# Performance work log

Measured on AMD Instinct MI355X. Metric: run time of the kernel, lower is better.

Reference implementation:

```python
import jax, jax.numpy as jnp
import numpy as np

T, H, I, E, S = 1024, 1024, 512, 64, 2  # tokens, hidden, intermediate, routed experts, shared experts
G, TOPK_GROUP, K = 8, 4, 8              # n_group, topk_group, num_experts_per_tok


def setup_inputs() -> dict:
    key = jax.random.key(0)
    ks = jax.random.split(key, 6)
    scale = 0.02
    x = jax.random.normal(ks[0], (T, H), dtype=jnp.float32)
    gate_w = jax.random.normal(ks[1], (E, H), dtype=jnp.float32) * scale   # MoEGate.weight [E,H]
    w_gu = jax.random.normal(ks[2], (E, H, 2 * I), dtype=jnp.float32) * scale  # gate_up_proj.weight.T per expert
    w_d = jax.random.normal(ks[3], (E, I, H), dtype=jnp.float32) * scale       # down_proj.weight.T per expert
    s_gu = jax.random.normal(ks[4], (S, H, 2 * I), dtype=jnp.float32) * scale  # shared experts
    s_d = jax.random.normal(ks[5], (S, I, H), dtype=jnp.float32) * scale
    return {"x": x, "gate_w": gate_w, "w_gu": w_gu, "w_d": w_d, "s_gu": s_gu, "s_d": s_d}


def _moe_forward(x, gate_w, w_gu, w_d, s_gu, s_d):
    t, h = x.shape
    e = w_gu.shape[0]
    i = w_gu.shape[2] // 2
    group_size = e // G

    # ---- shared experts (always active), summed ----
    sh = jnp.einsum('th,shf->stf', x, s_gu)            # [S,T,2I]
    shared = jnp.einsum('stf,sfh->th', jax.nn.silu(sh[..., :i]) * sh[..., i:], s_d)

    # ---- grouped top-k gating ----
    logits = x @ gate_w.T                               # [T,E]
    group_logits = logits.reshape(t, G, group_size)
    gw, gi = jax.lax.top_k(group_logits, TOPK_GROUP)    # [T,G,topk_group]
    gw = gw.reshape(t, G * TOPK_GROUP)
    gi = gi.reshape(t, G * TOPK_GROUP)
    topk_w, ti = jax.lax.top_k(gw, K)                   # [T,K]
    sel_group = ti // TOPK_GROUP
    expert_in_group = jnp.take_along_axis(gi, ti, axis=1)
    topk_idx = sel_group * group_size + expert_in_group # [T,K]
    topk_w = topk_w / (topk_w.sum(axis=-1, keepdims=True) + 1e-20)  # norm_topk_prob

    # ---- combine weights: sparse [T,E] scatter of top-k weights ----
    combine = jnp.zeros((t, e), x.dtype).at[jnp.arange(t)[:, None], topk_idx].add(topk_w)

    # ---- routed experts: dense grouped GEMM, zero-weighted where unselected ----
    gu = jnp.einsum('th,ehf->etf', x, w_gu)             # [E,T,2I]
    hidden = jax.nn.silu(gu[..., :i]) * gu[..., i:]     # [E,T,I]
    y = jnp.einsum('eti,eih->eth', hidden, w_d)         # [E,T,H]
    routed = jnp.einsum('eth,te->th', y, combine)

    return shared + routed


def reference(x, gate_w, w_gu, w_d, s_gu, s_d):
    return _moe_forward(x, gate_w, w_gu, w_d, s_gu, s_d)
```

## Files before the change

### kernel.cpp

```cpp
#include <hip/hip_runtime.h>
#include <hip/hip_bf16.h>

#define T_ 1024
#define H_ 1024
#define I_ 512
#define E_ 64
#define S_ 2
#define NJOB 66
#define KSEL 8
#define GRP 8
#define GSIZE 8
#define TKG 4
#define ROWS_TOTAL (T_*KSEL + S_*T_)

typedef __attribute__((ext_vector_type(8))) __bf16 bf16x8;
typedef __attribute__((ext_vector_type(8))) unsigned short u16x8;
typedef __attribute__((ext_vector_type(4))) unsigned short u16x4;
typedef __attribute__((ext_vector_type(4))) float f32x4;

__device__ inline unsigned short f2bf(float f) {
    unsigned u = __float_as_uint(f);
    u += 0x7FFFu + ((u >> 16) & 1u);
    return (unsigned short)(u >> 16);
}

__device__ inline unsigned pk2bf(float a, float b) {
    unsigned short ua = __builtin_bit_cast(unsigned short, (__bf16)a);
    unsigned short ub = __builtin_bit_cast(unsigned short, (__bf16)b);
    return (unsigned)ua | ((unsigned)ub << 16);
}

__device__ inline void async16(const void* g, void* l) {
    __builtin_amdgcn_global_load_lds(
        (const __attribute__((address_space(1))) unsigned int*)g,
        (__attribute__((address_space(3))) unsigned int*)(uintptr_t)l,
        16, 0, 0);
}

__global__ __launch_bounds__(256) void cvt_x_kernel(const float* __restrict__ x,
                                                    unsigned short* __restrict__ xb) {
    int i = (blockIdx.x * 256 + threadIdx.x) * 4;
    f32x4 v = *(const f32x4*)(x + i);
    u16x4 o;
    o[0] = f2bf(v[0]); o[1] = f2bf(v[1]); o[2] = f2bf(v[2]); o[3] = f2bf(v[3]);
    *(u16x4*)(xb + i) = o;
}

__global__ __launch_bounds__(256) void gate_kernel(const float* __restrict__ x,
                                                   const float* __restrict__ gate_w,
                                                   int* __restrict__ counts,
                                                   int* __restrict__ topk_idx,
                                                   float* __restrict__ topk_w) {
    __shared__ float Wt[64 * 65];
    __shared__ float Xs[4 * 65];
    __shared__ float lg[4 * 65];

    int tid = threadIdx.x;
    int t0 = blockIdx.x * 4;
    int e = tid & 63;
    int wq = tid >> 6;
    int er = tid >> 2;
    int kq = (tid & 3) * 16;
    int xk = tid & 63;

    float acc = 0.f;
    for (int kc = 0; kc < 16; ++kc) {
        const float* wp = gate_w + er * H_ + kc * 64 + kq;
        f32x4 w0 = *(const f32x4*)(wp);
        f32x4 w1 = *(const f32x4*)(wp + 4);
        f32x4 w2 = *(const f32x4*)(wp + 8);
        f32x4 w3 = *(const f32x4*)(wp + 12);
        float xv = x[(size_t)(t0 + wq) * H_ + kc * 64 + xk];
        __syncthreads();
#pragma unroll
        for (int i = 0; i < 4; ++i) {
            Wt[(kq + i) * 65 + er] = w0[i];
            Wt[(kq + 4 + i) * 65 + er] = w1[i];
            Wt[(kq + 8 + i) * 65 + er] = w2[i];
            Wt[(kq + 12 + i) * 65 + er] = w3[i];
        }
        Xs[wq * 65 + xk] = xv;
        __syncthreads();
#pragma unroll 8
        for (int k = 0; k < 64; ++k)
            acc += Wt[k * 65 + e] * Xs[wq * 65 + k];
    }
    lg[wq * 65 + e] = acc;
    __syncthreads();

    if (tid < 4) {
        int t = t0 + tid;
        const float* L = &lg[tid * 65];
        float cv[GRP * TKG];
        int   ce[GRP * TKG];
        for (int g = 0; g < GRP; ++g) {
            unsigned used = 0;
            for (int r = 0; r < TKG; ++r) {
                float best = -INFINITY; int bi = 0;
                for (int j = 0; j < GSIZE; ++j) {
                    if (used & (1u << j)) continue;
                    float v = L[g * GSIZE + j];
                    if (v > best) { best = v; bi = j; }
                }
                used |= 1u << bi;
                cv[g * TKG + r] = best;
                ce[g * TKG + r] = g * GSIZE + bi;
            }
        }
        float sv[KSEL]; int si[KSEL];
        unsigned used = 0;
        float sum = 0.0f;
        for (int r = 0; r < KSEL; ++r) {
            float best = -INFINITY; int bi = 0;
            for (int j = 0; j < GRP * TKG; ++j) {
                if (used & (1u << j)) continue;
                if (cv[j] > best) { best = cv[j]; bi = j; }
            }
            used |= 1u << bi;
            sv[r] = best; si[r] = ce[bi];
            sum += best;
        }
        float inv = 1.0f / (sum + 1e-20f);
        for (int r = 0; r < KSEL; ++r) {
            topk_idx[t * KSEL + r] = si[r];
            topk_w[t * KSEL + r] = sv[r] * inv;
            atomicAdd(&counts[si[r]], 1);
        }
    }
}

__global__ void prefix_kernel(int* __restrict__ counts, int* __restrict__ offsets,
                              int* __restrict__ cursor) {
    if (threadIdx.x == 0) {
        counts[E_] = T_;
        counts[E_ + 1] = T_;
        int acc = 0;
        for (int j = 0; j < NJOB; ++j) {
            offsets[j] = acc;
            cursor[j] = acc;
            acc += counts[j];
        }
        offsets[NJOB] = acc;
    }
}

__global__ __launch_bounds__(256) void place_kernel(const int* __restrict__ topk_idx,
                                                    const float* __restrict__ topk_w,
                                                    const int* __restrict__ offsets,
                                                    int* __restrict__ cursor,
                                                    int* __restrict__ row_token,
                                                    float* __restrict__ row_w) {
    int p = blockIdx.x * 256 + threadIdx.x;
    if (p < T_ * KSEL) {
        int t = p >> 3;
        int e = topk_idx[p];
        int slot = atomicAdd(&cursor[e], 1);
        row_token[slot] = t;
        row_w[slot] = topk_w[p];
    } else if (p < T_ * KSEL + S_ * T_) {
        int q = p - T_ * KSEL;
        int s = q >> 10;
        int t = q & (T_ - 1);
        int slot = offsets[E_ + s] + t;
        row_token[slot] = t;
        row_w[slot] = 1.0f;
    }
}

__global__ __launch_bounds__(256) void gateup_kernel(const unsigned short* __restrict__ xb,
                                                     const float* __restrict__ w_gu,
                                                     const float* __restrict__ s_gu,
                                                     const int* __restrict__ offsets,
                                                     const int* __restrict__ row_token,
                                                     unsigned short* __restrict__ hidden) {
    int job = blockIdx.x, mt = blockIdx.y, nt = blockIdx.z;
    int seg = offsets[job];
    int cnt = offsets[job + 1] - seg;
    int m0 = mt * 128;
    if (m0 >= cnt) return;
    const float* W = (job < E_) ? (w_gu + (size_t)job * H_ * (2 * I_))
                                : (s_gu + (size_t)(job - E_) * H_ * (2 * I_));
    int n0 = nt * 64;

    __shared__ unsigned short As[128 * 64];
    __shared__ unsigned short Bg[64 * 64];
    __shared__ unsigned short Bu[64 * 64];

    int tid = threadIdx.x;
    int wv = tid >> 6, lane = tid & 63, lrow = lane & 15, lq = lane >> 4;

    const unsigned short* asrc[4];
#pragma unroll
    for (int i = 0; i < 4; ++i) {
        int d = i * 256 + tid;
        int row = d >> 3;
        int kc = (d & 7) ^ (row & 7);
        int r = m0 + row;
        int gi = seg + (r < cnt ? r : 0);
        asrc[i] = xb + (size_t)row_token[gi] * H_ + kc * 8;
    }

    int bk = (tid & 15) * 4;
    int bn = (tid >> 4) * 4;
    int c0 = bk >> 3;
    int h8 = (bk & 4) * 2;
    const float* bbase = W + (size_t)bk * (2 * I_) + n0 + bn;

    f32x4 accg[2][4], accu[2][4];
    f32x4 zero = {0.f, 0.f, 0.f, 0.f};
#pragma unroll
    for (int a = 0; a < 2; ++a)
#pragma unroll
        for (int c = 0; c < 4; ++c) { accg[a][c] = zero; accu[a][c] = zero; }

    f32x4 g[4], u[4];
#pragma unroll
    for (int r = 0; r < 4; ++r) {
        g[r] = *(const f32x4*)(bbase + (size_t)r * (2 * I_));
        u[r] = *(const f32x4*)(bbase + (size_t)r * (2 * I_) + I_);
    }

    for (int kt = 0; kt < H_ / 64; ++kt) {
        int ko = kt * 64;
#pragma unroll
        for (int i = 0; i < 4; ++i)
            async16(asrc[i] + ko, &As[(i * 256 + tid) * 8]);

#pragma unroll
        for (int j = 0; j < 4; ++j) {
            int nj = bn + j;
            int byteoff = nj * 128 + ((c0 ^ (nj & 7)) * 16) + h8;
            uint2 vg, vu;
            vg.x = pk2bf(g[0][j], g[1][j]); vg.y = pk2bf(g[2][j], g[3][j]);
            vu.x = pk2bf(u[0][j], u[1][j]); vu.y = pk2bf(u[2][j], u[3][j]);
            *(uint2*)((char*)Bg + byteoff) = vg;
            *(uint2*)((char*)Bu + byteoff) = vu;
        }

        {
            int kn = ((kt + 1) & 15) * 64;
            const float* bp = bbase + (size_t)kn * (2 * I_);
#pragma unroll
            for (int r = 0; r < 4; ++r) {
                g[r] = *(const f32x4*)(bp + (size_t)r * (2 * I_));
                u[r] = *(const f32x4*)(bp + (size_t)r * (2 * I_) + I_);
            }
        }
        __syncthreads();

#pragma unroll
        for (int kk = 0; kk < 2; ++kk) {
            bf16x8 a[2];
#pragma unroll
            for (int rb = 0; rb < 2; ++rb) {
                int R = wv * 32 + rb * 16 + lrow;
                a[rb] = *(const bf16x8*)&As[R * 64 + (((lq + kk * 4) ^ (R & 7)) * 8)];
            }
#pragma unroll
            for (int cb = 0; cb < 4; ++cb) {
                int n = cb * 16 + lrow;
                int koff = ((lq + kk * 4) ^ (n & 7)) * 8;
                bf16x8 bg = *(const bf16x8*)&Bg[n * 64 + koff];
                bf16x8 bu = *(const bf16x8*)&Bu[n * 64 + koff];
#pragma unroll
                for (int rb = 0; rb < 2; ++rb) {
                    accg[rb][cb] = __builtin_amdgcn_mfma_f32_16x16x32_bf16(a[rb], bg, accg[rb][cb], 0, 0, 0);
                    accu[rb][cb] = __builtin_amdgcn_mfma_f32_16x16x32_bf16(a[rb], bu, accu[rb][cb], 0, 0, 0);
                }
            }
        }
        __syncthreads();
    }

#pragma unroll
    for (int rb = 0; rb < 2; ++rb)
#pragma unroll
        for (int cb = 0; cb < 4; ++cb)
#pragma unroll
            for (int r = 0; r < 4; ++r) {
                int row = wv * 32 + rb * 16 + lq * 4 + r;
                if (m0 + row < cnt) {
                    float gg = accg[rb][cb][r];
                    float uu = accu[rb][cb][r];
                    float hh = gg / (1.0f + __expf(-gg)) * uu;
                    hidden[(size_t)(seg + m0 + row) * I_ + n0 + cb * 16 + lrow] = f2bf(hh);
                }
            }
}

__global__ __launch_bounds__(256) void down_kernel(const unsigned short* __restrict__ hidden,
                                                   const float* __restrict__ w_d,
                                                   const float* __restrict__ s_d,
                                                   const int* __restrict__ offsets,
                                                   const int* __restrict__ row_token,
                                                   const float* __restrict__ row_w,
                                                   float* __restrict__ out) {
    int job = blockIdx.x, mt = blockIdx.y, nt = blockIdx.z;
    int seg = offsets[job];
    int cnt = offsets[job + 1] - seg;
    int m0 = mt * 128;
    if (m0 >= cnt) return;
    const float* W = (job < E_) ? (w_d + (size_t)job * I_ * H_)
                                : (s_d + (size_t)(job - E_) * I_ * H_);
    int n0 = nt * 64;

    __shared__ unsigned short As[128 * 64];
    __shared__ unsigned short Bs[64 * 64];

    int tid = threadIdx.x;
    int wv = tid >> 6, lane = tid & 63, lrow = lane & 15, lq = lane >> 4;

    const unsigned short* asrc[4];
#pragma unroll
    for (int i = 0; i < 4; ++i) {
        int d = i * 256 + tid;
        int row = d >> 3;
        int kc = (d & 7) ^ (row & 7);
        int r = m0 + row;
        int gi = seg + (r < cnt ? r : 0);
        asrc[i] = hidden + (size_t)gi * I_ + kc * 8;
    }

    int bk = (tid & 15) * 4;
    int bn = (tid >> 4) * 4;
    int c0 = bk >> 3;
    int h8 = (bk & 4) * 2;
    const float* bbase = W + (size_t)bk * H_ + n0 + bn;

    f32x4 acc[2][4];
    f32x4 zero = {0.f, 0.f, 0.f, 0.f};
#pragma unroll
    for (int a = 0; a < 2; ++a)
#pragma unroll
        for (int c = 0; c < 4; ++c) acc[a][c] = zero;

    f32x4 d4[4];
#pragma unroll
    for (int r = 0; r < 4; ++r)
        d4[r] = *(const f32x4*)(bbase + (size_t)r * H_);

    for (int kt = 0; kt < I_ / 64; ++kt) {
        int ko = kt * 64;
#pragma unroll
        for (int i = 0; i < 4; ++i)
            async16(asrc[i] + ko, &As[(i * 256 + tid) * 8]);

#pragma unroll
        for (int j = 0; j < 4; ++j) {
            int nj = bn + j;
            int byteoff = nj * 128 + ((c0 ^ (nj & 7)) * 16) + h8;
            uint2 vb;
            vb.x = pk2bf(d4[0][j], d4[1][j]); vb.y = pk2bf(d4[2][j], d4[3][j]);
            *(uint2*)((char*)Bs + byteoff) = vb;
        }
        {
            int kn = ((kt + 1) & 7) * 64;
            const float* bp = bbase + (size_t)kn * H_;
#pragma unroll
            for (int r = 0; r < 4; ++r)
                d4[r] = *(const f32x4*)(bp + (size_t)r * H_);
        }
        __syncthreads();

#pragma unroll
        for (int kk = 0; kk < 2; ++kk) {
            bf16x8 a[2];
#pragma unroll
            for (int rb = 0; rb < 2; ++rb) {
                int R = wv * 32 + rb * 16 + lrow;
                a[rb] = *(const bf16x8*)&As[R * 64 + (((lq + kk * 4) ^ (R & 7)) * 8)];
            }
#pragma unroll
            for (int cb = 0; cb < 4; ++cb) {
                int n = cb * 16 + lrow;
                bf16x8 b = *(const bf16x8*)&Bs[n * 64 + (((lq + kk * 4) ^ (n & 7)) * 8)];
#pragma unroll
                for (int rb = 0; rb < 2; ++rb)
                    acc[rb][cb] = __builtin_amdgcn_mfma_f32_16x16x32_bf16(a[rb], b, acc[rb][cb], 0, 0, 0);
            }
        }
        __syncthreads();
    }

#pragma unroll
    for (int rb = 0; rb < 2; ++rb)
#pragma unroll
        for (int r = 0; r < 4; ++r) {
            int row = wv * 32 + rb * 16 + lq * 4 + r;
            if (m0 + row < cnt) {
                int gi = seg + m0 + row;
                int tok = row_token[gi];
                float w = row_w[gi];
#pragma unroll
                for (int cb = 0; cb < 4; ++cb)
                    atomicAdd(&out[(size_t)tok * H_ + n0 + cb * 16 + lrow],
                              acc[rb][cb][r] * w);
            }
        }
}

extern "C" void kernel_launch(void* const* d_in, const int* in_sizes, int n_in,
                              void* d_out, int out_size, void* d_ws, size_t ws_size,
                              hipStream_t stream) {
    const float* x      = (const float*)d_in[0];
    const float* gate_w = (const float*)d_in[1];
    const float* w_gu   = (const float*)d_in[2];
    const float* w_d    = (const float*)d_in[3];
    const float* s_gu   = (const float*)d_in[4];
    const float* s_d    = (const float*)d_in[5];
    float* out = (float*)d_out;

    char* ws = (char*)d_ws;
    size_t off = 0;
    auto carve = [&](size_t bytes) -> void* {
        void* p = ws + off;
        off += (bytes + 255) & ~(size_t)255;
        return p;
    };
    int* counts            = (int*)carve(NJOB * 4);
    int* offsets           = (int*)carve((NJOB + 1) * 4);
    int* cursor            = (int*)carve(NJOB * 4);
    int* topk_idx          = (int*)carve(T_ * KSEL * 4);
    float* topk_w          = (float*)carve(T_ * KSEL * 4);
    int* row_token         = (int*)carve(ROWS_TOTAL * 4);
    float* row_w           = (float*)carve(ROWS_TOTAL * 4);
    unsigned short* xb     = (unsigned short*)carve((size_t)T_ * H_ * 2);
    unsigned short* hidden = (unsigned short*)carve((size_t)ROWS_TOTAL * I_ * 2);

    hipMemsetAsync(out, 0, (size_t)T_ * H_ * 4, stream);
    hipMemsetAsync(counts, 0, NJOB * 4, stream);

    cvt_x_kernel<<<(T_ * H_ / 4) / 256, 256, 0, stream>>>(x, xb);
    gate_kernel<<<T_ / 4, 256, 0, stream>>>(x, gate_w, counts, topk_idx, topk_w);
    prefix_kernel<<<1, 64, 0, stream>>>(counts, offsets, cursor);
    place_kernel<<<(ROWS_TOTAL + 255) / 256, 256, 0, stream>>>(topk_idx, topk_w, offsets,
                                                               cursor, row_token, row_w);
    gateup_kernel<<<dim3(NJOB, T_ / 128, I_ / 64), 256, 0, stream>>>(xb, w_gu, s_gu, offsets,
                                                                     row_token, hidden);
    down_kernel<<<dim3(NJOB, T_ / 128, H_ / 64), 256, 0, stream>>>(hidden, w_d, s_d, offsets,
                                                                   row_token, row_w, out);
}
```

Baseline: 626.3 us.

## Replace atomic scatter with per-row output buffer and reduce kernel; enlarge M tiles

The down-projection now writes unweighted per-row results to a dense yrow buffer, and a new reduce kernel gathers each token's eight routed rows plus both shared rows, applying the top-k weights. This removes the float atomicAdd scatter and the output memset. GEMM blocks grow to 256 rows with 512 threads, which halves how often each expert's weight tile is reloaded and converted. The prefix sum becomes a parallel scan. The cost is roughly 40 MB of extra yrow traffic, more LDS per block, and lower occupancy.

```diff
diff --git a/kernel.cpp b/kernel.cpp
--- a/kernel.cpp
+++ b/kernel.cpp
@@ -12,6 +12,8 @@
 #define GSIZE 8
 #define TKG 4
 #define ROWS_TOTAL (T_*KSEL + S_*T_)
+#define SH0 (T_*KSEL)
+#define SH1 (T_*KSEL + T_)
 
 typedef __attribute__((ext_vector_type(8))) __bf16 bf16x8;
 typedef __attribute__((ext_vector_type(8))) unsigned short u16x8;
@@ -129,45 +131,54 @@
     }
 }
 
-__global__ void prefix_kernel(int* __restrict__ counts, int* __restrict__ offsets,
-                              int* __restrict__ cursor) {
-    if (threadIdx.x == 0) {
-        counts[E_] = T_;
-        counts[E_ + 1] = T_;
-        int acc = 0;
-        for (int j = 0; j < NJOB; ++j) {
-            offsets[j] = acc;
-            cursor[j] = acc;
-            acc += counts[j];
-        }
-        offsets[NJOB] = acc;
-    }
+__global__ __launch_bounds__(128) void prefix_kernel(const int* __restrict__ counts,
+                                                     int* __restrict__ offsets,
+                                                     int* __restrict__ cursor) {
+    __shared__ int c[NJOB];
+    int tid = threadIdx.x;
+    int own = 0;
+    if (tid < NJOB) {
+        own = (tid < E_) ? counts[tid] : T_;
+        c[tid] = own;
+    }
+    __syncthreads();
+    for (int d = 1; d < NJOB; d <<= 1) {
+        int v = 0;
+        if (tid < NJOB && tid >= d) v = c[tid - d];
+        __syncthreads();
+        if (tid < NJOB) c[tid] += v;
+        __syncthreads();
+    }
+    if (tid < NJOB) {
+        int excl = c[tid] - own;
+        offsets[tid] = excl;
+        cursor[tid] = excl;
+    }
+    if (tid == 0) offsets[NJOB] = ROWS_TOTAL;
 }
 
 __global__ __launch_bounds__(256) void place_kernel(const int* __restrict__ topk_idx,
-                                                    const float* __restrict__ topk_w,
                                                     const int* __restrict__ offsets,
                                                     int* __restrict__ cursor,
                                                     int* __restrict__ row_token,
-                                                    float* __restrict__ row_w) {
+                                                    int* __restrict__ slot_map) {
     int p = blockIdx.x * 256 + threadIdx.x;
     if (p < T_ * KSEL) {
         int t = p >> 3;
         int e = topk_idx[p];
         int slot = atomicAdd(&cursor[e], 1);
         row_token[slot] = t;
-        row_w[slot] = topk_w[p];
+        slot_map[p] = slot;
     } else if (p < T_ * KSEL + S_ * T_) {
         int q = p - T_ * KSEL;
         int s = q >> 10;
         int t = q & (T_ - 1);
         int slot = offsets[E_ + s] + t;
         row_token[slot] = t;
-        row_w[slot] = 1.0f;
-    }
-}
-
-__global__ __launch_bounds__(256) void gateup_kernel(const unsigned short* __restrict__ xb,
+    }
+}
+
+__global__ __launch_bounds__(512) void gateup_kernel(const unsigned short* __restrict__ xb,
                                                      const float* __restrict__ w_gu,
                                                      const float* __restrict__ s_gu,
                                                      const int* __restrict__ offsets,
@@ -176,13 +187,13 @@
     int job = blockIdx.x, mt = blockIdx.y, nt = blockIdx.z;
     int seg = offsets[job];
     int cnt = offsets[job + 1] - seg;
-    int m0 = mt * 128;
+    int m0 = mt * 256;
     if (m0 >= cnt) return;
     const float* W = (job < E_) ? (w_gu + (size_t)job * H_ * (2 * I_))
                                 : (s_gu + (size_t)(job - E_) * H_ * (2 * I_));
     int n0 = nt * 64;
 
-    __shared__ unsigned short As[128 * 64];
+    __shared__ unsigned short As[256 * 64];
     __shared__ unsigned short Bg[64 * 64];
     __shared__ unsigned short Bu[64 * 64];
 
@@ -192,7 +203,7 @@
     const unsigned short* asrc[4];
 #pragma unroll
     for (int i = 0; i < 4; ++i) {
-        int d = i * 256 + tid;
+        int d = i * 512 + tid;
         int row = d >> 3;
         int kc = (d & 7) ^ (row & 7);
         int r = m0 + row;
@@ -200,10 +211,10 @@
         asrc[i] = xb + (size_t)row_token[gi] * H_ + kc * 8;
     }
 
-    int bk = (tid & 15) * 4;
-    int bn = (tid >> 4) * 4;
+    int bk = (tid & 31) * 2;
+    int bn = (tid >> 5) * 4;
     int c0 = bk >> 3;
-    int h8 = (bk & 4) * 2;
+    int hb = (bk & 7) * 2;
     const float* bbase = W + (size_t)bk * (2 * I_) + n0 + bn;
 
     f32x4 accg[2][4], accu[2][4];
@@ -213,9 +224,9 @@
 #pragma unroll
         for (int c = 0; c < 4; ++c) { accg[a][c] = zero; accu[a][c] = zero; }
 
-    f32x4 g[4], u[4];
-#pragma unroll
-    for (int r = 0; r < 4; ++r) {
+    f32x4 g[2], u[2];
+#pragma unroll
+    for (int r = 0; r < 2; ++r) {
         g[r] = *(const f32x4*)(bbase + (size_t)r * (2 * I_));
         u[r] = *(const f32x4*)(bbase + (size_t)r * (2 * I_) + I_);
     }
@@ -224,24 +235,21 @@
         int ko = kt * 64;
 #pragma unroll
         for (int i = 0; i < 4; ++i)
-            async16(asrc[i] + ko, &As[(i * 256 + tid) * 8]);
+            async16(asrc[i] + ko, &As[(i * 512 + tid) * 8]);
 
 #pragma unroll
         for (int j = 0; j < 4; ++j) {
             int nj = bn + j;
-            int byteoff = nj * 128 + ((c0 ^ (nj & 7)) * 16) + h8;
-            uint2 vg, vu;
-            vg.x = pk2bf(g[0][j], g[1][j]); vg.y = pk2bf(g[2][j], g[3][j]);
-            vu.x = pk2bf(u[0][j], u[1][j]); vu.y = pk2bf(u[2][j], u[3][j]);
-            *(uint2*)((char*)Bg + byteoff) = vg;
-            *(uint2*)((char*)Bu + byteoff) = vu;
+            int byteoff = nj * 128 + ((c0 ^ (nj & 7)) * 16) + hb;
+            *(unsigned*)((char*)Bg + byteoff) = pk2bf(g[0][j], g[1][j]);
+            *(unsigned*)((char*)Bu + byteoff) = pk2bf(u[0][j], u[1][j]);
         }
 
         {
             int kn = ((kt + 1) & 15) * 64;
             const float* bp = bbase + (size_t)kn * (2 * I_);
 #pragma unroll
-            for (int r = 0; r < 4; ++r) {
+            for (int r = 0; r < 2; ++r) {
                 g[r] = *(const f32x4*)(bp + (size_t)r * (2 * I_));
                 u[r] = *(const f32x4*)(bp + (size_t)r * (2 * I_) + I_);
             }
@@ -288,23 +296,21 @@
             }
 }
 
-__global__ __launch_bounds__(256) void down_kernel(const unsigned short* __restrict__ hidden,
+__global__ __launch_bounds__(512) void down_kernel(const unsigned short* __restrict__ hidden,
                                                    const float* __restrict__ w_d,
                                                    const float* __restrict__ s_d,
                                                    const int* __restrict__ offsets,
-                                                   const int* __restrict__ row_token,
-                                                   const float* __restrict__ row_w,
-                                                   float* __restrict__ out) {
+                                                   float* __restrict__ yrow) {
     int job = blockIdx.x, mt = blockIdx.y, nt = blockIdx.z;
     int seg = offsets[job];
     int cnt = offsets[job + 1] - seg;
-    int m0 = mt * 128;
+    int m0 = mt * 256;
     if (m0 >= cnt) return;
     const float* W = (job < E_) ? (w_d + (size_t)job * I_ * H_)
                                 : (s_d + (size_t)(job - E_) * I_ * H_);
     int n0 = nt * 64;
 
-    __shared__ unsigned short As[128 * 64];
+    __shared__ unsigned short As[256 * 64];
     __shared__ unsigned short Bs[64 * 64];
 
     int tid = threadIdx.x;
@@ -313,7 +319,7 @@
     const unsigned short* asrc[4];
 #pragma unroll
     for (int i = 0; i < 4; ++i) {
-        int d = i * 256 + tid;
+        int d = i * 512 + tid;
         int row = d >> 3;
         int kc = (d & 7) ^ (row & 7);
         int r = m0 + row;
@@ -321,10 +327,10 @@
         asrc[i] = hidden + (size_t)gi * I_ + kc * 8;
     }
 
-    int bk = (tid & 15) * 4;
-    int bn = (tid >> 4) * 4;
+    int bk = (tid & 31) * 2;
+    int bn = (tid >> 5) * 4;
     int c0 = bk >> 3;
-    int h8 = (bk & 4) * 2;
+    int hb = (bk & 7) * 2;
     const float* bbase = W + (size_t)bk * H_ + n0 + bn;
 
     f32x4 acc[2][4];
@@ -334,30 +340,28 @@
 #pragma unroll
         for (int c = 0; c < 4; ++c) acc[a][c] = zero;
 
-    f32x4 d4[4];
-#pragma unroll
-    for (int r = 0; r < 4; ++r)
+    f32x4 d4[2];
+#pragma unroll
+    for (int r = 0; r < 2; ++r)
         d4[r] = *(const f32x4*)(bbase + (size_t)r * H_);
 
     for (int kt = 0; kt < I_ / 64; ++kt) {
         int ko = kt * 64;
 #pragma unroll
         for (int i = 0; i < 4; ++i)
-            async16(asrc[i] + ko, &As[(i * 256 + tid) * 8]);
+            async16(asrc[i] + ko, &As[(i * 512 + tid) * 8]);
 
 #pragma unroll
         for (int j = 0; j < 4; ++j) {
             int nj = bn + j;
-            int byteoff = nj * 128 + ((c0 ^ (nj & 7)) * 16) + h8;
-            uint2 vb;
-            vb.x = pk2bf(d4[0][j], d4[1][j]); vb.y = pk2bf(d4[2][j], d4[3][j]);
-            *(uint2*)((char*)Bs + byteoff) = vb;
+            int byteoff = nj * 128 + ((c0 ^ (nj & 7)) * 16) + hb;
+            *(unsigned*)((char*)Bs + byteoff) = pk2bf(d4[0][j], d4[1][j]);
         }
         {
             int kn = ((kt + 1) & 7) * 64;
             const float* bp = bbase + (size_t)kn * H_;
 #pragma unroll
-            for (int r = 0; r < 4; ++r)
+            for (int r = 0; r < 2; ++r)
                 d4[r] = *(const f32x4*)(bp + (size_t)r * H_);
         }
         __syncthreads();
@@ -388,15 +392,39 @@
         for (int r = 0; r < 4; ++r) {
             int row = wv * 32 + rb * 16 + lq * 4 + r;
             if (m0 + row < cnt) {
-                int gi = seg + m0 + row;
-                int tok = row_token[gi];
-                float w = row_w[gi];
 #pragma unroll
                 for (int cb = 0; cb < 4; ++cb)
-                    atomicAdd(&out[(size_t)tok * H_ + n0 + cb * 16 + lrow],
-                              acc[rb][cb][r] * w);
-            }
-        }
+                    yrow[(size_t)(seg + m0 + row) * H_ + n0 + cb * 16 + lrow] = acc[rb][cb][r];
+            }
+        }
+}
+
+__global__ __launch_bounds__(256) void reduce_kernel(const float* __restrict__ yrow,
+                                                     const int* __restrict__ slot_map,
+                                                     const float* __restrict__ topk_w,
+                                                     float* __restrict__ out) {
+    int t = blockIdx.x;
+    __shared__ int sl[KSEL];
+    __shared__ float sw[KSEL];
+    if (threadIdx.x < KSEL) {
+        sl[threadIdx.x] = slot_map[t * KSEL + threadIdx.x];
+        sw[threadIdx.x] = topk_w[t * KSEL + threadIdx.x];
+    }
+    __syncthreads();
+    int col = threadIdx.x * 4;
+    f32x4 a0 = *(const f32x4*)(yrow + (size_t)(SH0 + t) * H_ + col);
+    f32x4 a1 = *(const f32x4*)(yrow + (size_t)(SH1 + t) * H_ + col);
+    f32x4 acc;
+#pragma unroll
+    for (int j = 0; j < 4; ++j) acc[j] = a0[j] + a1[j];
+#pragma unroll
+    for (int k = 0; k < KSEL; ++k) {
+        f32x4 v = *(const f32x4*)(yrow + (size_t)sl[k] * H_ + col);
+        float w = sw[k];
+#pragma unroll
+        for (int j = 0; j < 4; ++j) acc[j] += v[j] * w;
+    }
+    *(f32x4*)(out + (size_t)t * H_ + col) = acc;
 }
 
 extern "C" void kernel_launch(void* const* d_in, const int* in_sizes, int n_in,
@@ -423,20 +451,21 @@
     int* topk_idx          = (int*)carve(T_ * KSEL * 4);
     float* topk_w          = (float*)carve(T_ * KSEL * 4);
     int* row_token         = (int*)carve(ROWS_TOTAL * 4);
-    float* row_w           = (float*)carve(ROWS_TOTAL * 4);
+    int* slot_map          = (int*)carve(T_ * KSEL * 4);
     unsigned short* xb     = (unsigned short*)carve((size_t)T_ * H_ * 2);
     unsigned short* hidden = (unsigned short*)carve((size_t)ROWS_TOTAL * I_ * 2);
-
-    hipMemsetAsync(out, 0, (size_t)T_ * H_ * 4, stream);
+    float* yrow            = (float*)carve((size_t)ROWS_TOTAL * H_ * 4);
+
     hipMemsetAsync(counts, 0, NJOB * 4, stream);
 
     cvt_x_kernel<<<(T_ * H_ / 4) / 256, 256, 0, stream>>>(x, xb);
     gate_kernel<<<T_ / 4, 256, 0, stream>>>(x, gate_w, counts, topk_idx, topk_w);
-    prefix_kernel<<<1, 64, 0, stream>>>(counts, offsets, cursor);
-    place_kernel<<<(ROWS_TOTAL + 255) / 256, 256, 0, stream>>>(topk_idx, topk_w, offsets,
-                                                               cursor, row_token, row_w);
-    gateup_kernel<<<dim3(NJOB, T_ / 128, I_ / 64), 256, 0, stream>>>(xb, w_gu, s_gu, offsets,
+    prefix_kernel<<<1, 128, 0, stream>>>(counts, offsets, cursor);
+    place_kernel<<<(ROWS_TOTAL + 255) / 256, 256, 0, stream>>>(topk_idx, offsets,
+                                                               cursor, row_token, slot_map);
+    gateup_kernel<<<dim3(NJOB, T_ / 256, I_ / 64), 512, 0, stream>>>(xb, w_gu, s_gu, offsets,
                                                                      row_token, hidden);
-    down_kernel<<<dim3(NJOB, T_ / 128, H_ / 64), 256, 0, stream>>>(hidden, w_d, s_d, offsets,
-                                                                   row_token, row_w, out);
-}
+    down_kernel<<<dim3(NJOB, T_ / 256, H_ / 64), 512, 0, stream>>>(hidden, w_d, s_d, offsets,
+                                                                   yrow);
+    reduce_kernel<<<T_, 256, 0, stream>>>(yrow, slot_map, topk_w, out);
+}
```

Result: no change. 621.7 us (-0.7%).
